# Optimization experiments

Measured on AMD Instinct MI355X. Metric: run time of the kernel, lower is better.

The kernel has to match this reference:

```python
import jax, jax.numpy as jnp
import numpy as np

D_MODEL = 1024
NUM_HEADS = 16
D_HEAD = D_MODEL // NUM_HEADS
PATCH = 128


def setup_inputs() -> dict:
    key = jax.random.key(0)
    ks = jax.random.split(key, 10)
    B, T = 4, 8192
    x = jax.random.normal(ks[0], (B, T, D_MODEL), dtype=jnp.float32)
    coords = jax.random.uniform(ks[1], (B, T, 2), dtype=jnp.float32)
    s = 1.0 / np.sqrt(D_MODEL)
    Wq = jax.random.normal(ks[2], (D_MODEL, D_MODEL), dtype=jnp.float32) * s
    Wk = jax.random.normal(ks[3], (D_MODEL, D_MODEL), dtype=jnp.float32) * s
    Wv = jax.random.normal(ks[4], (D_MODEL, D_MODEL), dtype=jnp.float32) * s
    Wo = jax.random.normal(ks[5], (D_MODEL, D_MODEL), dtype=jnp.float32) * s
    bq = jnp.zeros((D_MODEL,), jnp.float32)
    bk = jnp.zeros((D_MODEL,), jnp.float32)
    bv = jnp.zeros((D_MODEL,), jnp.float32)
    bo = jnp.zeros((D_MODEL,), jnp.float32)
    return {"x": x, "coords": coords, "Wq": Wq, "bq": bq, "Wk": Wk, "bk": bk,
            "Wv": Wv, "bv": bv, "Wo": Wo, "bo": bo}


def _patched_attn(x, Wq, bq, Wk, bk, Wv, bv, Wo, bo):
    B, T, D = x.shape
    P = PATCH
    pad_len = (P - T % P) % P
    if pad_len > 0:
        x = jnp.pad(x, ((0, 0), (0, pad_len), (0, 0)))
    Tp = T + pad_len
    n = Tp // P
    xp = x.reshape(B * n, P, D)  # [N, P, D], independent patches
    def heads(y):  # [N, P, D] -> [N, H, P, dh]
        return y.reshape(B * n, P, NUM_HEADS, D_HEAD).transpose(0, 2, 1, 3)
    q = heads(xp @ Wq + bq)
    k = heads(xp @ Wk + bk)
    v = heads(xp @ Wv + bv)
    scores = jnp.einsum('bhtd,bhTd->bhtT', q, k) / jnp.sqrt(jnp.asarray(D_HEAD, x.dtype))
    w = jax.nn.softmax(scores, axis=-1)
    out = jnp.einsum('bhtT,bhTd->bhtd', w, v)
    out = out.transpose(0, 2, 1, 3).reshape(B * n, P, D)
    out = out @ Wo + bo
    out = out.reshape(B, Tp, D)
    if pad_len > 0:
        out = out[:, :T, :]
    return out


def reference(x, coords, Wq, bq, Wk, bk, Wv, bv, Wo, bo):
    # coords participates only in padding/reshape, not in the math
    return _patched_attn(x, Wq, bq, Wk, bk, Wv, bv, Wo, bo)
```

## Files before the change

### kernel.cpp

```cpp
#include <hip/hip_runtime.h>
#include <hip/hip_bf16.h>


#define DEV static __device__ __forceinline__

typedef __attribute__((ext_vector_type(8))) short short8;
typedef __attribute__((ext_vector_type(4))) float f32x4;

DEV unsigned short f2b(float f) {
  unsigned u = __builtin_bit_cast(unsigned, f);
  u += 0x7fffu + ((u >> 16) & 1u);
  return (unsigned short)(u >> 16);
}

DEV void load_lds16(const void* g, void* l) {
  __builtin_amdgcn_global_load_lds(
      (const __attribute__((address_space(1))) void*)g,
      (__attribute__((address_space(3))) void*)l, 16, 0, 0);
}

#define MFMA_BF16(a, b, c) __builtin_amdgcn_mfma_f32_16x16x32_bf16((a), (b), (c), 0, 0, 0)


__global__ void cvt_x_k(const float* __restrict__ x, unsigned short* __restrict__ xb, int n4) {
  int i = blockIdx.x * blockDim.x + threadIdx.x;
  int stride = gridDim.x * blockDim.x;
  for (; i < n4; i += stride) {
    float4 v = ((const float4*)x)[i];
    ushort4 o;
    o.x = f2b(v.x); o.y = f2b(v.y); o.z = f2b(v.z); o.w = f2b(v.w);
    ((ushort4*)xb)[i] = o;
  }
}

__global__ void twk4(const float* __restrict__ W0, const float* __restrict__ W1,
                     const float* __restrict__ W2, const float* __restrict__ W3,
                     unsigned short* __restrict__ Dqkv, unsigned short* __restrict__ Dot) {
  __shared__ unsigned short tile[64][65];
  const int w = blockIdx.x >> 8;
  const int t = blockIdx.x & 255;
  const float* W = (w == 0) ? W0 : (w == 1) ? W1 : (w == 2) ? W2 : W3;
  unsigned short* Wt = (w == 3) ? Dot : Dqkv + (size_t)w * 1024 * 1024;
  int k0 = (t >> 4) << 6;
  int n0 = (t & 15) << 6;
  int tx = threadIdx.x & 63;
  int ty = threadIdx.x >> 6;
#pragma unroll
  for (int i = 0; i < 16; ++i) {
    int r = (i << 2) + ty;
    tile[r][tx] = f2b(W[(size_t)(k0 + r) * 1024 + n0 + tx]);
  }
  __syncthreads();
#pragma unroll
  for (int i = 0; i < 16; ++i) {
    int n = (i << 2) + ty;
    Wt[(size_t)(n0 + n) * 1024 + k0 + tx] = tile[tx][n];
  }
}

__global__ void fuse_bias_k(const float* __restrict__ bq, const float* __restrict__ bk,
                            const float* __restrict__ bv, float* __restrict__ bqkv) {
  int i = blockIdx.x * 256 + threadIdx.x;
  if (i < 1024) bqkv[i] = bq[i];
  else if (i < 2048) bqkv[i] = bk[i - 1024];
  else if (i < 3072) bqkv[i] = bv[i - 2048];
}


template <bool OUT_F32>
__global__ __launch_bounds__(256)
void gemm_bt(const unsigned short* __restrict__ A,
             const unsigned short* __restrict__ Bt,
             const float* __restrict__ bias,
             void* __restrict__ Cv, int M, int N, int K) {
  __shared__ __align__(16) unsigned short sA[128 * 32];
  __shared__ __align__(16) unsigned short sB[128 * 32];

  int nwg = gridDim.x;
  int bid = blockIdx.x;
  int wg = bid;
  if ((nwg & 7) == 0) {
    int cpx = nwg >> 3;
    wg = (bid & 7) * cpx + (bid >> 3);
  }
  const int nbn = N >> 7;
  const int bm = wg / nbn;
  const int bn = wg - bm * nbn;

  const int tid = threadIdx.x;
  const int lane = tid & 63;
  const int wv = tid >> 6;
  const int wr = wv >> 1, wc = wv & 1;
  const int fr = lane & 15;
  const int fks = (lane >> 4) << 3;

  const int srow = tid >> 2;
  const int scol = (tid & 3) << 3;
  const unsigned short* gA = A + (size_t)(bm * 128 + srow) * K + scol;
  const unsigned short* gB = Bt + (size_t)(bn * 128 + srow) * K + scol;
  unsigned short* lA = sA + (wv << 9);
  unsigned short* lB = sB + (wv << 9);

  const unsigned short* pa = sA + (wr * 64 + fr) * 32 + fks;
  const unsigned short* pb = sB + (wc * 64 + fr) * 32 + fks;

  f32x4 acc[4][4] = {};

  for (int k0 = 0; k0 < K; k0 += 32) {
    load_lds16(gA + k0, lA);
    load_lds16(gA + (size_t)64 * K + k0, lA + 2048);
    load_lds16(gB + k0, lB);
    load_lds16(gB + (size_t)64 * K + k0, lB + 2048);
    __syncthreads();
    short8 af[4], bfv[4];
#pragma unroll
    for (int i = 0; i < 4; ++i) af[i] = *(const short8*)(pa + i * 512);
#pragma unroll
    for (int i = 0; i < 4; ++i) bfv[i] = *(const short8*)(pb + i * 512);
#pragma unroll
    for (int i = 0; i < 4; ++i)
#pragma unroll
      for (int j = 0; j < 4; ++j)
        acc[i][j] = MFMA_BF16(af[i], bfv[j], acc[i][j]);
    __syncthreads();
  }

  const int grow0 = bm * 128 + wr * 64 + ((lane >> 4) << 2);
  const int gcol0 = bn * 128 + wc * 64 + fr;
#pragma unroll
  for (int j = 0; j < 4; ++j) {
    const int gc = gcol0 + j * 16;
    const float bv_ = bias[gc];
#pragma unroll
    for (int i = 0; i < 4; ++i) {
      const int gr = grow0 + i * 16;
#pragma unroll
      for (int r = 0; r < 4; ++r) {
        float v = acc[i][j][r] + bv_;
        if (OUT_F32) ((float*)Cv)[(size_t)(gr + r) * N + gc] = v;
        else ((unsigned short*)Cv)[(size_t)(gr + r) * N + gc] = f2b(v);
      }
    }
  }
}


__global__ __launch_bounds__(256)
void attn_k(const unsigned short* __restrict__ qkv, unsigned short* __restrict__ out) {
  const int bh = blockIdx.x;
  const int p = bh >> 4, h = bh & 15;
  const int tid = threadIdx.x, lane = tid & 63, wv = tid >> 6;
  const int fr = lane & 15, fks = (lane >> 4) << 3;

  __shared__ __align__(16) unsigned short vt[64][136];
  __shared__ __align__(16) unsigned short pls[4][32][136];

  const size_t rowbase = (size_t)p * 128 * 3072;

  {
    const unsigned short* vsrc = qkv + rowbase + 2048 + (size_t)h * 64;
#pragma unroll
    for (int it = 0; it < 8; ++it) {
      int idx = tid + it * 256;
      int t = idx >> 4;
      int d4 = (idx & 15) << 2;
      ushort4 vv = *(const ushort4*)(vsrc + (size_t)t * 3072 + d4);
      vt[d4 + 0][t] = vv.x; vt[d4 + 1][t] = vv.y;
      vt[d4 + 2][t] = vv.z; vt[d4 + 3][t] = vv.w;
    }
  }

  short8 qf[2][2];
  {
    const unsigned short* qsrc = qkv + rowbase + (size_t)(wv * 32) * 3072 + h * 64;
#pragma unroll
    for (int mf = 0; mf < 2; ++mf)
#pragma unroll
      for (int kc = 0; kc < 2; ++kc)
        qf[mf][kc] = *(const short8*)(qsrc + (size_t)(mf * 16 + fr) * 3072 + kc * 32 + fks);
  }

  f32x4 s[2][8] = {};
  {
    const unsigned short* ksrc = qkv + rowbase + 1024 + (size_t)h * 64;
#pragma unroll
    for (int kc = 0; kc < 2; ++kc)
#pragma unroll
      for (int nf = 0; nf < 8; ++nf) {
        short8 kf = *(const short8*)(ksrc + (size_t)(nf * 16 + fr) * 3072 + kc * 32 + fks);
        s[0][nf] = MFMA_BF16(qf[0][kc], kf, s[0][nf]);
        s[1][nf] = MFMA_BF16(qf[1][kc], kf, s[1][nf]);
      }
  }
  __syncthreads();

  const float c0 = 0.125f * 1.44269504088896f;
  float sm[2][4];
#pragma unroll
  for (int mf = 0; mf < 2; ++mf)
#pragma unroll
    for (int r = 0; r < 4; ++r) {
      float m = s[mf][0][r];
#pragma unroll
      for (int nf = 1; nf < 8; ++nf) m = fmaxf(m, s[mf][nf][r]);
      m = fmaxf(m, __shfl_xor(m, 1));
      m = fmaxf(m, __shfl_xor(m, 2));
      m = fmaxf(m, __shfl_xor(m, 4));
      m = fmaxf(m, __shfl_xor(m, 8));
      float su = 0.f;
#pragma unroll
      for (int nf = 0; nf < 8; ++nf) {
        float e = exp2f((s[mf][nf][r] - m) * c0);
        s[mf][nf][r] = e;
        su += e;
      }
      su += __shfl_xor(su, 1);
      su += __shfl_xor(su, 2);
      su += __shfl_xor(su, 4);
      su += __shfl_xor(su, 8);
      sm[mf][r] = su;
    }

#pragma unroll
  for (int mf = 0; mf < 2; ++mf)
#pragma unroll
    for (int nf = 0; nf < 8; ++nf)
#pragma unroll
      for (int r = 0; r < 4; ++r)
        pls[wv][mf * 16 + ((lane >> 4) << 2) + r][nf * 16 + fr] = f2b(s[mf][nf][r]);

  f32x4 o[2][4] = {};
#pragma unroll
  for (int kc = 0; kc < 4; ++kc) {
    short8 pf0 = *(const short8*)&pls[wv][fr][kc * 32 + fks];
    short8 pf1 = *(const short8*)&pls[wv][16 + fr][kc * 32 + fks];
#pragma unroll
    for (int nf = 0; nf < 4; ++nf) {
      short8 vf = *(const short8*)&vt[nf * 16 + fr][kc * 32 + fks];
      o[0][nf] = MFMA_BF16(pf0, vf, o[0][nf]);
      o[1][nf] = MFMA_BF16(pf1, vf, o[1][nf]);
    }
  }

  unsigned short* obase = out + (size_t)(p * 128 + wv * 32) * 1024 + h * 64;
#pragma unroll
  for (int mf = 0; mf < 2; ++mf)
#pragma unroll
    for (int nf = 0; nf < 4; ++nf)
#pragma unroll
      for (int r = 0; r < 4; ++r) {
        int row = mf * 16 + ((lane >> 4) << 2) + r;
        float val = o[mf][nf][r] / sm[mf][r];
        obase[(size_t)row * 1024 + nf * 16 + fr] = f2b(val);
      }
}


extern "C" void kernel_launch(void* const* d_in, const int* in_sizes, int n_in,
                              void* d_out, int out_size, void* d_ws, size_t ws_size,
                              hipStream_t stream) {
  const float* x  = (const float*)d_in[0];
  const float* Wq = (const float*)d_in[2];
  const float* bq = (const float*)d_in[3];
  const float* Wk = (const float*)d_in[4];
  const float* bk = (const float*)d_in[5];
  const float* Wv = (const float*)d_in[6];
  const float* bv = (const float*)d_in[7];
  const float* Wo = (const float*)d_in[8];
  const float* bo = (const float*)d_in[9];

  char* ws = (char*)d_ws;
  unsigned short* xb   = (unsigned short*)(ws);
  unsigned short* wqkv = (unsigned short*)(ws + 67108864);
  unsigned short* wot  = (unsigned short*)(ws + 73400320);
  float*          bqkv = (float*)(ws + 75497472);
  unsigned short* qkv  = (unsigned short*)(ws + 75509760);

  cvt_x_k<<<2048, 256, 0, stream>>>(x, xb, (32768 * 1024) / 4);
  twk4<<<1024, 256, 0, stream>>>(Wq, Wk, Wv, Wo, wqkv, wot);
  fuse_bias_k<<<12, 256, 0, stream>>>(bq, bk, bv, bqkv);

  gemm_bt<false><<<6144, 256, 0, stream>>>(xb, wqkv, bqkv, qkv, 32768, 3072, 1024);
  attn_k<<<4096, 256, 0, stream>>>(qkv, xb);
  gemm_bt<true><<<2048, 256, 0, stream>>>(xb, wot, bo, d_out, 32768, 1024, 1024);
}
```

Measured before the change: 718.5 us.

## Replace 128x128 GEMM with double-buffered 256x256 swizzled-LDS GEMM kernel

Both projection GEMMs now use a new kernel with 512 threads and a 256x256 output tile. It uses a K-step of 64 and double-buffers LDS, prefetching the next tile with direct global-to-LDS loads while the current one computes. LDS rows are XOR-swizzled to avoid bank conflicts, and the MFMA phases run under raised wave priority. This aims to raise data reuse per load and hide memory latency, in exchange for 128KB of LDS per block, heavy register use for a 32-fragment accumulator, and fewer workgroups.

```diff
diff --git a/kernel.cpp b/kernel.cpp
--- a/kernel.cpp
+++ b/kernel.cpp
@@ -68,71 +68,104 @@
 
 
 template <bool OUT_F32>
-__global__ __launch_bounds__(256)
-void gemm_bt(const unsigned short* __restrict__ A,
+__global__ __launch_bounds__(512, 2)
+void gemm256(const unsigned short* __restrict__ A,
              const unsigned short* __restrict__ Bt,
              const float* __restrict__ bias,
              void* __restrict__ Cv, int M, int N, int K) {
-  __shared__ __align__(16) unsigned short sA[128 * 32];
-  __shared__ __align__(16) unsigned short sB[128 * 32];
-
-  int nwg = gridDim.x;
-  int bid = blockIdx.x;
-  int wg = bid;
+  __shared__ __align__(16) unsigned short sh[65536];
+
+  int nwg = gridDim.x, bid = blockIdx.x, wg = bid;
   if ((nwg & 7) == 0) {
     int cpx = nwg >> 3;
     wg = (bid & 7) * cpx + (bid >> 3);
   }
-  const int nbn = N >> 7;
-  const int bm = wg / nbn;
-  const int bn = wg - bm * nbn;
-
-  const int tid = threadIdx.x;
-  const int lane = tid & 63;
-  const int wv = tid >> 6;
-  const int wr = wv >> 1, wc = wv & 1;
-  const int fr = lane & 15;
-  const int fks = (lane >> 4) << 3;
-
-  const int srow = tid >> 2;
-  const int scol = (tid & 3) << 3;
-  const unsigned short* gA = A + (size_t)(bm * 128 + srow) * K + scol;
-  const unsigned short* gB = Bt + (size_t)(bn * 128 + srow) * K + scol;
-  unsigned short* lA = sA + (wv << 9);
-  unsigned short* lB = sB + (wv << 9);
-
-  const unsigned short* pa = sA + (wr * 64 + fr) * 32 + fks;
-  const unsigned short* pb = sB + (wc * 64 + fr) * 32 + fks;
-
-  f32x4 acc[4][4] = {};
-
-  for (int k0 = 0; k0 < K; k0 += 32) {
-    load_lds16(gA + k0, lA);
-    load_lds16(gA + (size_t)64 * K + k0, lA + 2048);
-    load_lds16(gB + k0, lB);
-    load_lds16(gB + (size_t)64 * K + k0, lB + 2048);
-    __syncthreads();
-    short8 af[4], bfv[4];
-#pragma unroll
-    for (int i = 0; i < 4; ++i) af[i] = *(const short8*)(pa + i * 512);
-#pragma unroll
-    for (int i = 0; i < 4; ++i) bfv[i] = *(const short8*)(pb + i * 512);
-#pragma unroll
-    for (int i = 0; i < 4; ++i)
-#pragma unroll
-      for (int j = 0; j < 4; ++j)
-        acc[i][j] = MFMA_BF16(af[i], bfv[j], acc[i][j]);
-    __syncthreads();
-  }
-
-  const int grow0 = bm * 128 + wr * 64 + ((lane >> 4) << 2);
-  const int gcol0 = bn * 128 + wc * 64 + fr;
+  const int nbn = N >> 8;
+  const int bm = wg / nbn, bn = wg - bm * nbn;
+
+  const int tid = threadIdx.x, lane = tid & 63, w = tid >> 6;
+  const int wm = w >> 2, wn = w & 3;
+  const int fr = lane & 15, g = lane >> 4;
+
+  const int lr = lane >> 3;
+  const int lb = ((lane & 7) << 4) ^ (lr << 4);
+  const unsigned short* gsrc = (w < 4)
+      ? A  + (size_t)(bm * 256 + w * 64 + lr) * K + (lb >> 1)
+      : Bt + (size_t)(bn * 256 + (w - 4) * 64 + lr) * K + (lb >> 1);
+  const int ldsw = w * 8192;
+
+  const int koff0 = (g * 16) ^ ((fr & 7) << 4);
+  const int koff1 = koff0 ^ 64;
+
+  f32x4 acc[8][4] = {};
+  const int NT = K >> 6;
+
+  {
+    char* l0 = (char*)sh + ldsw;
+#pragma unroll
+    for (int c = 0; c < 8; ++c)
+      load_lds16(gsrc + (size_t)c * 8 * K, l0 + c * 1024);
+  }
+
+  for (int t = 0; t < NT; ++t) {
+    if (t + 1 < NT) {
+      const unsigned short* sN = gsrc + (size_t)(t + 1) * 64;
+      char* lN = (char*)sh + ((t + 1) & 1) * 65536 + ldsw;
+#pragma unroll
+      for (int c = 0; c < 8; ++c)
+        load_lds16(sN + (size_t)c * 8 * K, lN + c * 1024);
+      asm volatile("s_waitcnt vmcnt(8)" ::: "memory");
+    } else {
+      asm volatile("s_waitcnt vmcnt(0)" ::: "memory");
+    }
+    __builtin_amdgcn_sched_barrier(0);
+    __builtin_amdgcn_s_barrier();
+
+    const char* bufp = (const char*)sh + (t & 1) * 65536;
+    const char* ap0 = bufp + (wm * 128 + fr) * 128;
+    const char* bp0 = bufp + 32768 + (wn * 64 + fr) * 128;
+
+#pragma unroll
+    for (int q = 0; q < 4; ++q) {
+      const int mh = q >> 1, nh = q & 1;
+      short8 af[4][2], bf[2][2];
+      const char* ap = ap0 + mh * 64 * 128;
+      const char* bp = bp0 + nh * 32 * 128;
+#pragma unroll
+      for (int ii = 0; ii < 4; ++ii) {
+        af[ii][0] = *(const short8*)(ap + ii * 2048 + koff0);
+        af[ii][1] = *(const short8*)(ap + ii * 2048 + koff1);
+      }
+#pragma unroll
+      for (int jj = 0; jj < 2; ++jj) {
+        bf[jj][0] = *(const short8*)(bp + jj * 2048 + koff0);
+        bf[jj][1] = *(const short8*)(bp + jj * 2048 + koff1);
+      }
+      __builtin_amdgcn_s_barrier();
+      asm volatile("s_waitcnt lgkmcnt(0)" ::: "memory");
+      __builtin_amdgcn_sched_barrier(0);
+      __builtin_amdgcn_s_setprio(1);
+#pragma unroll
+      for (int s = 0; s < 2; ++s)
+#pragma unroll
+        for (int ii = 0; ii < 4; ++ii)
+#pragma unroll
+          for (int jj = 0; jj < 2; ++jj)
+            acc[mh * 4 + ii][nh * 2 + jj] =
+                MFMA_BF16(af[ii][s], bf[jj][s], acc[mh * 4 + ii][nh * 2 + jj]);
+      __builtin_amdgcn_s_setprio(0);
+      __builtin_amdgcn_s_barrier();
+    }
+  }
+
+  const int grow0 = bm * 256 + wm * 128 + g * 4;
+  const int gcol0 = bn * 256 + wn * 64 + fr;
 #pragma unroll
   for (int j = 0; j < 4; ++j) {
     const int gc = gcol0 + j * 16;
     const float bv_ = bias[gc];
 #pragma unroll
-    for (int i = 0; i < 4; ++i) {
+    for (int i = 0; i < 8; ++i) {
       const int gr = grow0 + i * 16;
 #pragma unroll
       for (int r = 0; r < 4; ++r) {
@@ -280,7 +313,7 @@
   twk4<<<1024, 256, 0, stream>>>(Wq, Wk, Wv, Wo, wqkv, wot);
   fuse_bias_k<<<12, 256, 0, stream>>>(bq, bk, bv, bqkv);
 
-  gemm_bt<false><<<6144, 256, 0, stream>>>(xb, wqkv, bqkv, qkv, 32768, 3072, 1024);
+  gemm256<false><<<1536, 512, 0, stream>>>(xb, wqkv, bqkv, qkv, 32768, 3072, 1024);
   attn_k<<<4096, 256, 0, stream>>>(qkv, xb);
-  gemm_bt<true><<<2048, 256, 0, stream>>>(xb, wot, bo, d_out, 32768, 1024, 1024);
-}
+  gemm256<true><<<512, 512, 0, stream>>>(xb, wot, bo, d_out, 32768, 1024, 1024);
+}
```

After: 718.7 us. No clear change (+0.0%).
